# Performance work log

Hardware: AMD Instinct MI355X
Metric: run time of the kernel (lower is better)

The kernel has to match this reference:

```python
import jax, jax.numpy as jnp
import numpy as np

B, H, W, C = 8, 256, 256, 128  # batch, grid-H, grid-W, channel width
MODES = 16
SCALE = 1.0 / (C * C)  # 1/(in_width*out_width)


def _corner_mask(h, w, f):
    # mask truncates the FIRST two axes of w_ft (as in the original code),
    # keeping the full rfft axis.
    m = np.zeros((h, w, f), dtype=np.float32)
    m[:MODES, :MODES, :] = 1.0
    m[-MODES:, :MODES, :] = 1.0
    m[:MODES, -MODES:, :] = 1.0
    m[-MODES:, -MODES:, :] = 1.0
    return jnp.asarray(m)


def setup_inputs() -> dict:
    key = jax.random.key(0)
    k1, k2 = jax.random.split(key)
    x = jax.random.normal(k1, (B, H, W, C), dtype=jnp.float32)
    w = SCALE * jax.random.uniform(k2, (H, W, C), dtype=jnp.float32)
    b = jnp.zeros((H, W, C), dtype=jnp.float32)
    return {"x": x, "w": w, "b": b}


def reference(x, w, b):
    # rfft2d over the innermost two dims (W, C), matching tf.signal.rfft2d
    x_ft = jnp.fft.rfft2(x, axes=(-2, -1))   # [B, H, W, C//2+1] complex
    w_ft = jnp.fft.rfft2(w, axes=(-2, -1))   # [H, W, C//2+1]
    b_ft = jnp.fft.rfft2(b, axes=(-2, -1))
    xw_ft = x_ft * w_ft + b_ft               # broadcast over batch
    mask = _corner_mask(*w_ft.shape)         # corners along axes (0,1)
    xw_ft = xw_ft * mask
    # irfft2d with default sizes recovers last dim = 2*(C//2+1-1) = C
    return jnp.fft.irfft2(xw_ft, axes=(-2, -1))
```

## Files before the change

kernel.cpp:

```cpp
#include <hip/hip_runtime.h>

#define TPK 512
#define TPA 1024
#define NF0 512
#define FPB 5
#define NST (FPB * 8)

typedef float f4v __attribute__((ext_vector_type(4)));

__device__ __forceinline__ int br7(int k) {
  return (int)(__brev((unsigned int)k) >> 25);
}

__device__ __forceinline__ void bar_lds() {
  asm volatile("s_waitcnt lgkmcnt(0)\ns_barrier" ::: "memory");
}

#define FILL3(PT)                                                           \
  {                                                                         \
    _Pragma("unroll")                                                       \
    for (int _j = 0; _j < 3; ++_j) {                                        \
      const int _idx = 3 * (PT) + _j;                                       \
      if (_idx < NST) {                                                     \
        const int _zi = NF0 + bid * FPB + (_idx >> 3);                      \
        const int _zb = _zi / 224;                                          \
        const int _zh = 16 + (_zi - _zb * 224);                             \
        f4v* _o4 = (f4v*)(out + ((size_t)(_zb * 256 + _zh)) * 32768);       \
        __builtin_nontemporal_store(z, &_o4[tid + ((_idx & 7) << 10)]);     \
      }                                                                     \
    }                                                                       \
  }

template <int NT>
__device__ __forceinline__ void zero_fill_slab(float* __restrict__ out,
                                               int zi, int tid) {
  const int zb = zi / 224;
  const int zh = 16 + (zi - zb * 224);
  f4v* o4 = (f4v*)(out + ((size_t)(zb * 256 + zh)) * 32768);
  const f4v z = {0.f, 0.f, 0.f, 0.f};
  #pragma unroll 4
  for (int i = tid; i < 8192; i += NT)
    __builtin_nontemporal_store(z, &o4[i]);
}

__device__ __forceinline__ void fft16_pos(float* ar, float* ai) {
  constexpr float TC[4][8] = {
    {1.f, 0.f, 0.f, 0.f, 0.f, 0.f, 0.f, 0.f},
    {1.f, 0.f, 0.f, 0.f, 0.f, 0.f, 0.f, 0.f},
    {1.f, 0.70710678f, 0.f, -0.70710678f, 0.f, 0.f, 0.f, 0.f},
    {1.f, 0.92387953f, 0.70710678f, 0.38268343f, 0.f, -0.38268343f, -0.70710678f, -0.92387953f}
  };
  constexpr float TS[4][8] = {
    {0.f, 0.f, 0.f, 0.f, 0.f, 0.f, 0.f, 0.f},
    {0.f, 1.f, 0.f, 0.f, 0.f, 0.f, 0.f, 0.f},
    {0.f, 0.70710678f, 1.f, 0.70710678f, 0.f, 0.f, 0.f, 0.f},
    {0.f, 0.38268343f, 0.70710678f, 0.92387953f, 1.f, 0.92387953f, 0.70710678f, 0.38268343f}
  };
  #pragma unroll
  for (int s = 0; s < 4; ++s) {
    const int L = 1 << s;
    #pragma unroll
    for (int jj = 0; jj < 8; ++jj) {
      if (jj < L) {
        const float tc = TC[s][jj], ts = TS[s][jj];
        #pragma unroll
        for (int i0 = jj; i0 < 16; i0 += 2 * L) {
          const float xr = ar[i0 + L], xi = ai[i0 + L];
          const float pr = xr * tc - xi * ts;
          const float pi = xr * ts + xi * tc;
          const float qr = ar[i0], qi = ai[i0];
          ar[i0 + L] = qr - pr; ai[i0 + L] = qi - pi;
          ar[i0]     = qr + pr; ai[i0]     = qi + pi;
        }
      }
    }
  }
}

template <int TPBv>
__device__ void phaseA_reduce(const float* __restrict__ src,
                              float (*XR)[128], float (*XI)[128],
                              float (*SR)[128], float (*SI)[128],
                              const float* Rc, const float* Rs, int tid) {
  constexpr int NQ = TPBv / 128;
  constexpr int JN = 16 / NQ;
  const int c = tid & 127;
  const int q = tid >> 7;

  constexpr float C16[16] = {1.f, 0.92387953f, 0.70710678f, 0.38268343f, 0.f,
                             -0.38268343f, -0.70710678f, -0.92387953f, -1.f,
                             -0.92387953f, -0.70710678f, -0.38268343f, 0.f,
                             0.38268343f, 0.70710678f, 0.92387953f};
  constexpr float S16[16] = {0.f, 0.38268343f, 0.70710678f, 0.92387953f, 1.f,
                             0.92387953f, 0.70710678f, 0.38268343f, 0.f,
                             -0.38268343f, -0.70710678f, -0.92387953f, -1.f,
                             -0.92387953f, -0.70710678f, -0.38268343f};

  float accR[17], accI[17];
  #pragma unroll
  for (int f = 0; f < 17; ++f) { accR[f] = 0.f; accI[f] = 0.f; }

  #pragma unroll
  for (int j = 0; j < JN; ++j) {
    const int w0 = q * JN + j;
    float xv[16];
    #pragma unroll
    for (int w1 = 0; w1 < 16; ++w1)
      xv[w1] = src[(w1 * 16 + w0) * 128 + c];
    float SRe[9], SIm[9];
    #pragma unroll
    for (int g = 0; g < 9; ++g) {
      float sr = 0.f, si = 0.f;
      #pragma unroll
      for (int w1 = 0; w1 < 16; ++w1) {
        const int m = (g * w1) & 15;
        sr = fmaf(xv[w1], C16[m], sr);
        si = fmaf(xv[w1], -S16[m], si);
      }
      SRe[g] = sr; SIm[g] = si;
    }
    #pragma unroll
    for (int f = 0; f < 17; ++f) {
      const int g = f & 15;
      const float sr = (g <= 8) ? SRe[g] : SRe[16 - g];
      const float si = (g <= 8) ? SIm[g] : -SIm[16 - g];
      const int idx = (f * w0) & 255;
      const float tc = Rc[idx], ts = -Rs[idx];
      accR[f] = fmaf(sr, tc, fmaf(-si, ts, accR[f]));
      accI[f] = fmaf(sr, ts, fmaf(si, tc, accI[f]));
    }
  }
  #pragma unroll
  for (int r = 0; r < NQ / 2; ++r) {
    if (q == 2 * r) {
      if (r == 0) {
        #pragma unroll
        for (int f = 0; f < 17; ++f) { XR[f][c] = accR[f]; XI[f][c] = accI[f]; }
      } else {
        #pragma unroll
        for (int f = 0; f < 17; ++f) { XR[f][c] += accR[f]; XI[f][c] += accI[f]; }
      }
    } else if (q == 2 * r + 1) {
      if (r == 0) {
        #pragma unroll
        for (int f = 0; f < 17; ++f) { SR[f][c] = accR[f]; SI[f][c] = accI[f]; }
      } else {
        #pragma unroll
        for (int f = 0; f < 17; ++f) { SR[f][c] += accR[f]; SI[f][c] += accI[f]; }
      }
    }
    __syncthreads();
  }
  for (int u = tid; u < 17 * 128; u += TPBv) {
    const int row = u >> 7, cc = u & 127;
    XR[row][cc] += SR[row][cc];
    XI[row][cc] += SI[row][cc];
  }
  __syncthreads();
}

template <int TPBv>
__device__ void fftc17_lds(float (*XR)[128], float (*XI)[128],
                           const float* Rc, const float* Rs, int tid) {
  for (int s = 6; s >= 0; --s) {
    const int L = 1 << s;
    for (int u = tid; u < 17 * 64; u += TPBv) {
      const int row = u >> 6, qq = u & 63;
      const int jj = qq & (L - 1);
      const int pos = ((qq >> s) << (s + 1)) | jj;
      const int ti = jj << (7 - s);
      const float tc = Rc[ti], ts = Rs[ti];
      const float a0r = XR[row][pos],     a0i = XI[row][pos];
      const float b0r = XR[row][pos + L], b0i = XI[row][pos + L];
      XR[row][pos] = a0r + b0r; XI[row][pos] = a0i + b0i;
      const float dr = a0r - b0r, di = a0i - b0i;
      XR[row][pos + L] = fmaf(dr, tc, di * ts);
      XI[row][pos + L] = fmaf(di, tc, -dr * ts);
    }
    __syncthreads();
  }
}

__global__ __launch_bounds__(TPK) void k0_wft_and_fill(
    const float* __restrict__ wp, const float* __restrict__ bp,
    float2* __restrict__ wsW, float2* __restrict__ wsB,
    float* __restrict__ out) {
  const int bid = blockIdx.x;
  const int tid = threadIdx.x;
  if (bid >= 64) {
    zero_fill_slab<TPK>(out, bid - 64, tid);
    return;
  }
  __shared__ float XR[17][128], XI[17][128];
  __shared__ float SR[17][128], SI[17][128];
  __shared__ float Rc[256], Rs[256];
  for (int i = tid; i < 256; i += TPK) {
    float sv, cv; sincosf(6.283185307179586f * (float)i / 256.0f, &sv, &cv);
    Rc[i] = cv; Rs[i] = sv;
  }
  __syncthreads();
  const int which = bid >> 5;
  const int ha = bid & 31;
  const int h = (ha < 16) ? ha : (224 + ha);
  const float* src = (which ? bp : wp) + (size_t)h * 32768;
  phaseA_reduce<TPK>(src, XR, XI, SR, SI, Rc, Rs, tid);
  fftc17_lds<TPK>(XR, XI, Rc, Rs, tid);
  float2* dst = which ? wsB : wsW;
  for (int u = tid; u < 32 * 65; u += TPK) {
    const int fi = u / 65, k = u - fi * 65;
    const int f = fi - 16;
    float xr, xi;
    if (f >= 0) { const int p = br7(k); xr = XR[f][p]; xi = XI[f][p]; }
    else { const int kk = (128 - k) & 127; const int p = br7(kk);
           xr = XR[-f][p]; xi = -XI[-f][p]; }
    dst[(ha * 32 + fi) * 65 + k] = make_float2(xr, xi);
  }
}

__global__ __launch_bounds__(TPA, 4) void fourier_active(
    const float* __restrict__ x, const float2* __restrict__ wsW,
    const float2* __restrict__ wsB, float* __restrict__ out) {
  const int bid = blockIdx.x;
  const int tid = threadIdx.x;
  __shared__ float XR[17][128], XI[17][128];
  __shared__ float TR[32][128], TI[32][128];
  __shared__ float Rc[256], Rs[256];
  for (int i = tid; i < 256; i += TPA) {
    float sv, cv; sincosf(6.283185307179586f * (float)i / 256.0f, &sv, &cv);
    Rc[i] = cv; Rs[i] = sv;
  }
  __syncthreads();

  const int b = bid >> 5;
  const int ha = bid & 31;
  const int h = (ha < 16) ? ha : (224 + ha);
  const float* src = x + ((size_t)(b * 256 + h)) * 32768;
  phaseA_reduce<TPA>(src, XR, XI, (float(*)[128])TR, (float(*)[128])TI,
                     Rc, Rs, tid);

  float wfx[4], wfy[4], bfx[4], bfy[4];
  #pragma unroll
  for (int t = 0; t < 4; ++t) {
    const int u = tid + t * TPA;
    const int fi = u >> 7, k = u & 127;
    if (k <= 64) {
      const float2 wf = wsW[(ha * 32 + fi) * 65 + k];
      const float2 bf = wsB[(ha * 32 + fi) * 65 + k];
      wfx[t] = wf.x; wfy[t] = wf.y; bfx[t] = bf.x; bfy[t] = bf.y;
    } else { wfx[t] = 0.f; wfy[t] = 0.f; bfx[t] = 0.f; bfy[t] = 0.f; }
  }
  __builtin_amdgcn_sched_barrier(0);

  const f4v z = {0.f, 0.f, 0.f, 0.f};

  #pragma unroll
  for (int s = 6; s >= 0; --s) {
    const int L = 1 << s;
    for (int u = tid; u < 17 * 64; u += TPA) {
      const int row = u >> 6, qq = u & 63;
      const int jj = qq & (L - 1);
      const int pos = ((qq >> s) << (s + 1)) | jj;
      const int ti = jj << (7 - s);
      const float tc = Rc[ti], ts = Rs[ti];
      const float a0r = XR[row][pos],     a0i = XI[row][pos];
      const float b0r = XR[row][pos + L], b0i = XI[row][pos + L];
      XR[row][pos] = a0r + b0r; XI[row][pos] = a0i + b0i;
      const float dr = a0r - b0r, di = a0i - b0i;
      XR[row][pos + L] = fmaf(dr, tc, di * ts);
      XI[row][pos + L] = fmaf(di, tc, -dr * ts);
    }
    FILL3(6 - s);
    bar_lds();
  }

  #pragma unroll
  for (int t = 0; t < 4; ++t) {
    const int u = tid + t * TPA;
    const int fi = u >> 7, k = u & 127;
    float gr = 0.f, gi = 0.f;
    if (k <= 64) {
      const int f = fi - 16;
      float xr, xi;
      if (f >= 0) { const int p = br7(k); xr = XR[f][p]; xi = XI[f][p]; }
      else { const int kk = (128 - k) & 127; const int p = br7(kk);
             xr = XR[-f][p]; xi = -XI[-f][p]; }
      gr = xr * wfx[t] - xi * wfy[t] + bfx[t];
      gi = xr * wfy[t] + xi * wfx[t] + bfy[t];
      const float al = (k == 0 || k == 64) ? 1.f : 2.f;
      gr *= al; gi *= al;
    }
    const int p = br7(k);
    TR[fi][p] = gr; TI[fi][p] = gi;
  }
  FILL3(7);
  bar_lds();

  #pragma unroll
  for (int s = 0; s <= 6; ++s) {
    const int L = 1 << s;
    for (int u = tid; u < 32 * 64; u += TPA) {
      const int row = u >> 6, qq = u & 63;
      const int jj = qq & (L - 1);
      const int pos = ((qq >> s) << (s + 1)) | jj;
      const int ti = jj << (7 - s);
      const float tc = Rc[ti], ts = Rs[ti];
      const float b0r = TR[row][pos + L], b0i = TI[row][pos + L];
      const float pr = b0r * tc - b0i * ts;
      const float pi = fmaf(b0r, ts, b0i * tc);
      const float a0r = TR[row][pos], a0i = TI[row][pos];
      TR[row][pos + L] = a0r - pr; TI[row][pos + L] = a0i - pi;
      TR[row][pos]     = a0r + pr; TI[row][pos]     = a0i + pi;
    }
    FILL3(8 + s);
    bar_lds();
  }

  const int c = tid & 127;
  const int q = tid >> 7;
  constexpr int BR4[16] = {0, 8, 4, 12, 2, 10, 6, 14, 1, 9, 5, 13, 3, 11, 7, 15};
  const float inv = 1.0f / 32768.0f;
  float* og = out + ((size_t)(b * 256 + h)) * 32768;

  #pragma unroll 1
  for (int it = 0; it < 2; ++it) {
    const int w0 = q + it * 8;
    float Ur[16], Ui[16];
    #pragma unroll
    for (int g = 0; g < 16; ++g) {
      const int gb = BR4[g];
      const float t1r = TR[gb + 16][c], t1i = TI[gb + 16][c];
      const float t0r = TR[gb][c],      t0i = TI[gb][c];
      const int iw1 = (gb * w0) & 255;
      const int iw2 = ((gb - 16) * w0) & 255;
      const float c1 = Rc[iw1], s1 = Rs[iw1];
      const float c2 = Rc[iw2], s2 = Rs[iw2];
      Ur[g] = t1r * c1 - t1i * s1 + t0r * c2 - t0i * s2;
      Ui[g] = t1r * s1 + t1i * c1 + t0r * s2 + t0i * c2;
    }
    fft16_pos(Ur, Ui);
    #pragma unroll
    for (int w1 = 0; w1 < 16; ++w1)
      og[(w1 * 16 + w0) * 128 + c] = Ur[w1] * inv;
  }
}

extern "C" void kernel_launch(void* const* d_in, const int* in_sizes, int n_in,
                              void* d_out, int out_size, void* d_ws, size_t ws_size,
                              hipStream_t stream) {
  const float* x = (const float*)d_in[0];
  const float* w = (const float*)d_in[1];
  const float* b = (const float*)d_in[2];
  float* out = (float*)d_out;
  float2* wsW = (float2*)d_ws;
  float2* wsB = wsW + 32 * 32 * 65;

  hipLaunchKernelGGL(k0_wft_and_fill, dim3(64 + NF0), dim3(TPK), 0, stream,
                     w, b, wsW, wsB, out);
  hipLaunchKernelGGL(fourier_active, dim3(256), dim3(TPA), 0, stream,
                     x, wsW, wsB, out);
}
```

Before: 69.08 us.

## Warp-specialize main kernel: dedicated zero-fill waves plus register-based first-stage DFT

Splits each 1024-thread block so that 256 threads only issue nontemporal zero stores for the inactive output slabs, with their barrier count matched to the compute threads. The other 768 threads do the FFT work. The phase-A reduction is replaced by an inline per-thread 16-point DFT with twiddle accumulation and a staged LDS reduction. The weight and bias spectra are now loaded inside the multiply loop instead of prefetched. The zero-fill work is rebalanced toward the main kernel (NF0 512→256, 6 slabs per block), aiming to overlap the store traffic with compute, at the cost of fewer compute threads and a fragile barrier-count matching scheme.

New measurement: 70.56 us. +2.1%, slower.

```diff
diff --git a/kernel.cpp b/kernel.cpp
--- a/kernel.cpp
+++ b/kernel.cpp
@@ -2,9 +2,11 @@
 
 #define TPK 512
 #define TPA 1024
-#define NF0 512
-#define FPB 5
-#define NST (FPB * 8)
+#define CTH 768
+#define FPB 6
+#define NF0 256
+#define NACT 256
+#define NBAR 19
 
 typedef float f4v __attribute__((ext_vector_type(4)));
 
@@ -15,21 +17,6 @@
 __device__ __forceinline__ void bar_lds() {
   asm volatile("s_waitcnt lgkmcnt(0)\ns_barrier" ::: "memory");
 }
-
-#define FILL3(PT)                                                           \
-  {                                                                         \
-    _Pragma("unroll")                                                       \
-    for (int _j = 0; _j < 3; ++_j) {                                        \
-      const int _idx = 3 * (PT) + _j;                                       \
-      if (_idx < NST) {                                                     \
-        const int _zi = NF0 + bid * FPB + (_idx >> 3);                      \
-        const int _zb = _zi / 224;                                          \
-        const int _zh = 16 + (_zi - _zb * 224);                             \
-        f4v* _o4 = (f4v*)(out + ((size_t)(_zb * 256 + _zh)) * 32768);       \
-        __builtin_nontemporal_store(z, &_o4[tid + ((_idx & 7) << 10)]);     \
-      }                                                                     \
-    }                                                                       \
-  }
 
 template <int NT>
 __device__ __forceinline__ void zero_fill_slab(float* __restrict__ out,
@@ -38,9 +25,9 @@
   const int zh = 16 + (zi - zb * 224);
   f4v* o4 = (f4v*)(out + ((size_t)(zb * 256 + zh)) * 32768);
   const f4v z = {0.f, 0.f, 0.f, 0.f};
-  #pragma unroll 4
-  for (int i = tid; i < 8192; i += NT)
-    __builtin_nontemporal_store(z, &o4[i]);
+  #pragma unroll
+  for (int i = 0; i < 8192 / NT; ++i)
+    __builtin_nontemporal_store(z, &o4[tid + i * NT]);
 }
 
 __device__ __forceinline__ void fft16_pos(float* ar, float* ai) {
@@ -217,7 +204,7 @@
   }
 }
 
-__global__ __launch_bounds__(TPA, 4) void fourier_active(
+__global__ __launch_bounds__(TPA) void fourier_main(
     const float* __restrict__ x, const float2* __restrict__ wsW,
     const float2* __restrict__ wsB, float* __restrict__ out) {
   const int bid = blockIdx.x;
@@ -229,34 +216,120 @@
     float sv, cv; sincosf(6.283185307179586f * (float)i / 256.0f, &sv, &cv);
     Rc[i] = cv; Rs[i] = sv;
   }
-  __syncthreads();
-
+  bar_lds();
+
+  if (tid >= CTH) {
+    const int ftid = tid - CTH;
+    const f4v z = {0.f, 0.f, 0.f, 0.f};
+    #pragma unroll 1
+    for (int p = 0; p < NBAR; ++p) {
+      #pragma unroll
+      for (int j = 0; j < 11; ++j) {
+        const int idx = p * 11 + j;
+        if (idx < FPB * 32) {
+          const int s = idx >> 5;
+          const int zi = NF0 + bid * FPB + s;
+          const int zb = zi / 224;
+          const int zh = 16 + (zi - zb * 224);
+          f4v* o4 = (f4v*)(out + ((size_t)(zb * 256 + zh)) * 32768);
+          __builtin_nontemporal_store(z, &o4[((idx & 31) << 8) + ftid]);
+        }
+      }
+      bar_lds();
+    }
+    return;
+  }
+
+  const int c = tid & 127;
+  const int q = tid >> 7;
   const int b = bid >> 5;
   const int ha = bid & 31;
   const int h = (ha < 16) ? ha : (224 + ha);
   const float* src = x + ((size_t)(b * 256 + h)) * 32768;
-  phaseA_reduce<TPA>(src, XR, XI, (float(*)[128])TR, (float(*)[128])TI,
-                     Rc, Rs, tid);
-
-  float wfx[4], wfy[4], bfx[4], bfy[4];
-  #pragma unroll
-  for (int t = 0; t < 4; ++t) {
-    const int u = tid + t * TPA;
-    const int fi = u >> 7, k = u & 127;
-    if (k <= 64) {
-      const float2 wf = wsW[(ha * 32 + fi) * 65 + k];
-      const float2 bf = wsB[(ha * 32 + fi) * 65 + k];
-      wfx[t] = wf.x; wfy[t] = wf.y; bfx[t] = bf.x; bfy[t] = bf.y;
-    } else { wfx[t] = 0.f; wfy[t] = 0.f; bfx[t] = 0.f; bfy[t] = 0.f; }
-  }
-  __builtin_amdgcn_sched_barrier(0);
-
-  const f4v z = {0.f, 0.f, 0.f, 0.f};
-
-  #pragma unroll
+
+  {
+    constexpr float C16[16] = {1.f, 0.92387953f, 0.70710678f, 0.38268343f, 0.f,
+                               -0.38268343f, -0.70710678f, -0.92387953f, -1.f,
+                               -0.92387953f, -0.70710678f, -0.38268343f, 0.f,
+                               0.38268343f, 0.70710678f, 0.92387953f};
+    constexpr float S16[16] = {0.f, 0.38268343f, 0.70710678f, 0.92387953f, 1.f,
+                               0.92387953f, 0.70710678f, 0.38268343f, 0.f,
+                               -0.38268343f, -0.70710678f, -0.92387953f, -1.f,
+                               -0.92387953f, -0.70710678f, -0.38268343f};
+    const int jn = (q < 4) ? 3 : 2;
+    const int w0base = (q < 4) ? 3 * q : 12 + 2 * (q - 4);
+    float accR[17], accI[17];
+    #pragma unroll
+    for (int f = 0; f < 17; ++f) { accR[f] = 0.f; accI[f] = 0.f; }
+    #pragma unroll
+    for (int j = 0; j < 3; ++j) {
+      if (j < jn) {
+        const int w0 = w0base + j;
+        float xv[16];
+        #pragma unroll
+        for (int w1 = 0; w1 < 16; ++w1)
+          xv[w1] = src[(w1 * 16 + w0) * 128 + c];
+        float SRe[9], SIm[9];
+        #pragma unroll
+        for (int g = 0; g < 9; ++g) {
+          float sr = 0.f, si = 0.f;
+          #pragma unroll
+          for (int w1 = 0; w1 < 16; ++w1) {
+            const int m = (g * w1) & 15;
+            sr = fmaf(xv[w1], C16[m], sr);
+            si = fmaf(xv[w1], -S16[m], si);
+          }
+          SRe[g] = sr; SIm[g] = si;
+        }
+        #pragma unroll
+        for (int f = 0; f < 17; ++f) {
+          const int g = f & 15;
+          const float sr = (g <= 8) ? SRe[g] : SRe[16 - g];
+          const float si = (g <= 8) ? SIm[g] : -SIm[16 - g];
+          const int idx = (f * w0) & 255;
+          const float tc = Rc[idx], ts = -Rs[idx];
+          accR[f] = fmaf(sr, tc, fmaf(-si, ts, accR[f]));
+          accI[f] = fmaf(sr, ts, fmaf(si, tc, accI[f]));
+        }
+      }
+    }
+    float (*SR)[128] = (float(*)[128])TR;
+    float (*SI)[128] = (float(*)[128])TI;
+    if (q == 0) {
+      #pragma unroll
+      for (int f = 0; f < 17; ++f) { XR[f][c] = accR[f]; XI[f][c] = accI[f]; }
+    } else if (q == 1) {
+      #pragma unroll
+      for (int f = 0; f < 17; ++f) { SR[f][c] = accR[f]; SI[f][c] = accI[f]; }
+    }
+    bar_lds();
+    if (q == 2) {
+      #pragma unroll
+      for (int f = 0; f < 17; ++f) { XR[f][c] += accR[f]; XI[f][c] += accI[f]; }
+    } else if (q == 3) {
+      #pragma unroll
+      for (int f = 0; f < 17; ++f) { SR[f][c] += accR[f]; SI[f][c] += accI[f]; }
+    }
+    bar_lds();
+    if (q == 4) {
+      #pragma unroll
+      for (int f = 0; f < 17; ++f) { XR[f][c] += accR[f]; XI[f][c] += accI[f]; }
+    } else if (q == 5) {
+      #pragma unroll
+      for (int f = 0; f < 17; ++f) { SR[f][c] += accR[f]; SI[f][c] += accI[f]; }
+    }
+    bar_lds();
+    for (int u = tid; u < 17 * 128; u += CTH) {
+      const int row = u >> 7, cc = u & 127;
+      XR[row][cc] += SR[row][cc];
+      XI[row][cc] += SI[row][cc];
+    }
+    bar_lds();
+  }
+
   for (int s = 6; s >= 0; --s) {
     const int L = 1 << s;
-    for (int u = tid; u < 17 * 64; u += TPA) {
+    for (int u = tid; u < 17 * 64; u += CTH) {
       const int row = u >> 6, qq = u & 63;
       const int jj = qq & (L - 1);
       const int pos = ((qq >> s) << (s + 1)) | jj;
@@ -269,13 +342,10 @@
       XR[row][pos + L] = fmaf(dr, tc, di * ts);
       XI[row][pos + L] = fmaf(di, tc, -dr * ts);
     }
-    FILL3(6 - s);
-    bar_lds();
-  }
-
-  #pragma unroll
-  for (int t = 0; t < 4; ++t) {
-    const int u = tid + t * TPA;
+    bar_lds();
+  }
+
+  for (int u = tid; u < 32 * 128; u += CTH) {
     const int fi = u >> 7, k = u & 127;
     float gr = 0.f, gi = 0.f;
     if (k <= 64) {
@@ -284,21 +354,21 @@
       if (f >= 0) { const int p = br7(k); xr = XR[f][p]; xi = XI[f][p]; }
       else { const int kk = (128 - k) & 127; const int p = br7(kk);
              xr = XR[-f][p]; xi = -XI[-f][p]; }
-      gr = xr * wfx[t] - xi * wfy[t] + bfx[t];
-      gi = xr * wfy[t] + xi * wfx[t] + bfy[t];
+      const float2 wf = wsW[(ha * 32 + fi) * 65 + k];
+      const float2 bf = wsB[(ha * 32 + fi) * 65 + k];
+      gr = xr * wf.x - xi * wf.y + bf.x;
+      gi = xr * wf.y + xi * wf.x + bf.y;
       const float al = (k == 0 || k == 64) ? 1.f : 2.f;
       gr *= al; gi *= al;
     }
     const int p = br7(k);
     TR[fi][p] = gr; TI[fi][p] = gi;
   }
-  FILL3(7);
   bar_lds();
 
-  #pragma unroll
   for (int s = 0; s <= 6; ++s) {
     const int L = 1 << s;
-    for (int u = tid; u < 32 * 64; u += TPA) {
+    for (int u = tid; u < 32 * 64; u += CTH) {
       const int row = u >> 6, qq = u & 63;
       const int jj = qq & (L - 1);
       const int pos = ((qq >> s) << (s + 1)) | jj;
@@ -311,36 +381,35 @@
       TR[row][pos + L] = a0r - pr; TI[row][pos + L] = a0i - pi;
       TR[row][pos]     = a0r + pr; TI[row][pos]     = a0i + pi;
     }
-    FILL3(8 + s);
-    bar_lds();
-  }
-
-  const int c = tid & 127;
-  const int q = tid >> 7;
+    bar_lds();
+  }
+
   constexpr int BR4[16] = {0, 8, 4, 12, 2, 10, 6, 14, 1, 9, 5, 13, 3, 11, 7, 15};
   const float inv = 1.0f / 32768.0f;
   float* og = out + ((size_t)(b * 256 + h)) * 32768;
 
   #pragma unroll 1
-  for (int it = 0; it < 2; ++it) {
-    const int w0 = q + it * 8;
-    float Ur[16], Ui[16];
-    #pragma unroll
-    for (int g = 0; g < 16; ++g) {
-      const int gb = BR4[g];
-      const float t1r = TR[gb + 16][c], t1i = TI[gb + 16][c];
-      const float t0r = TR[gb][c],      t0i = TI[gb][c];
-      const int iw1 = (gb * w0) & 255;
-      const int iw2 = ((gb - 16) * w0) & 255;
-      const float c1 = Rc[iw1], s1 = Rs[iw1];
-      const float c2 = Rc[iw2], s2 = Rs[iw2];
-      Ur[g] = t1r * c1 - t1i * s1 + t0r * c2 - t0i * s2;
-      Ui[g] = t1r * s1 + t1i * c1 + t0r * s2 + t0i * c2;
-    }
-    fft16_pos(Ur, Ui);
-    #pragma unroll
-    for (int w1 = 0; w1 < 16; ++w1)
-      og[(w1 * 16 + w0) * 128 + c] = Ur[w1] * inv;
+  for (int it = 0; it < 3; ++it) {
+    const int w0 = q + 6 * it;
+    if (w0 < 16) {
+      float Ur[16], Ui[16];
+      #pragma unroll
+      for (int g = 0; g < 16; ++g) {
+        const int gb = BR4[g];
+        const float t1r = TR[gb + 16][c], t1i = TI[gb + 16][c];
+        const float t0r = TR[gb][c],      t0i = TI[gb][c];
+        const int iw1 = (gb * w0) & 255;
+        const int iw2 = ((gb - 16) * w0) & 255;
+        const float c1 = Rc[iw1], s1 = Rs[iw1];
+        const float c2 = Rc[iw2], s2 = Rs[iw2];
+        Ur[g] = t1r * c1 - t1i * s1 + t0r * c2 - t0i * s2;
+        Ui[g] = t1r * s1 + t1i * c1 + t0r * s2 + t0i * c2;
+      }
+      fft16_pos(Ur, Ui);
+      #pragma unroll
+      for (int w1 = 0; w1 < 16; ++w1)
+        og[(w1 * 16 + w0) * 128 + c] = Ur[w1] * inv;
+    }
   }
 }
 
@@ -356,6 +425,6 @@
 
   hipLaunchKernelGGL(k0_wft_and_fill, dim3(64 + NF0), dim3(TPK), 0, stream,
                      w, b, wsW, wsB, out);
-  hipLaunchKernelGGL(fourier_active, dim3(256), dim3(TPA), 0, stream,
+  hipLaunchKernelGGL(fourier_main, dim3(NACT), dim3(TPA), 0, stream,
                      x, wsW, wsB, out);
 }
```
